# Kernel optimization log

Hardware: AMD Instinct MI355X
Metric: run time of the kernel (lower is better)

Reference implementation:

```python
import jax, jax.numpy as jnp
import numpy as np

B, N, FN, FE, H, FC, OUT = 64, 32, 32, 16, 32, 128, 1
ENN_LAYERS, S2S_STEPS = 3, 3


def setup_inputs() -> dict:
    key = jax.random.key(0)
    ks = jax.random.split(key, 16)
    s = 0.1
    return {
        "x": jax.random.uniform(ks[0], (B, N, FN), dtype=jnp.float32),
        "edge": jax.random.normal(ks[1], (B, N, N, FE), dtype=jnp.float32),
        "adjacency": jax.random.randint(ks[2], (B, N, N), 0, 2).astype(jnp.float32),
        # embedding layer
        "W_emb": s * jax.random.normal(ks[3], (FN, H)),
        "b_emb": jnp.zeros((H,), jnp.float32),
        # edge MLP: FE -> FC -> H*H
        "W1": s * jax.random.normal(ks[4], (FE, FC)),
        "b1": jnp.zeros((FC,), jnp.float32),
        "W2": s * jax.random.normal(ks[5], (FC, H * H)),
        "b2": jnp.zeros((H * H,), jnp.float32),
        # GRU (torch layout: weight_ih [3H,H], weight_hh [3H,H])
        "gru_Wi": s * jax.random.normal(ks[6], (3 * H, H)),
        "gru_Wh": s * jax.random.normal(ks[7], (3 * H, H)),
        "gru_bi": jnp.zeros((3 * H,), jnp.float32),
        "gru_bh": jnp.zeros((3 * H,), jnp.float32),
        # Set2Set LSTM: input 2H, hidden H (torch layout weight_ih [4H,2H])
        "lstm_Wi": s * jax.random.normal(ks[8], (4 * H, 2 * H)),
        "lstm_Wh": s * jax.random.normal(ks[9], (4 * H, H)),
        "lstm_bi": jnp.zeros((4 * H,), jnp.float32),
        "lstm_bh": jnp.zeros((4 * H,), jnp.float32),
        # output fc: 2H -> OUT
        "Wf": s * jax.random.normal(ks[10], (2 * H, OUT)),
        "bf": jnp.zeros((OUT,), jnp.float32),
    }


def reference(x, edge, adjacency, W_emb, b_emb, W1, b1, W2, b2,
              gru_Wi, gru_Wh, gru_bi, gru_bh,
              lstm_Wi, lstm_Wh, lstm_bi, lstm_bh, Wf, bf):
    Bx, Nx, _ = x.shape
    Hd = W_emb.shape[1]
    # node mask: (sum over raw features > 0), [B,N,1]
    msk = (jnp.sum(x, axis=2, keepdims=True) > 0).astype(x.dtype)
    h = x @ W_emb + b_emb  # [B,N,H]
    # per-edge weight matrices from edge MLP (same every layer in the original)
    ew = (jax.nn.relu(edge @ W1 + b1) @ W2 + b2).reshape(Bx, Nx, Nx, Hd, Hd)
    for _ in range(ENN_LAYERS):
        # msg[b,i,j,:] = ew[b,i,j] @ h[b,i]; masked by adjacency, summed over source i
        m = jnp.einsum('bijuv,biv->biju', ew, h) * adjacency[..., None]
        m = m.sum(axis=1)  # [B,N,H]
        # single-step GRU (torch gate order r,z,n)
        gi = m @ gru_Wi.T + gru_bi
        gh = h @ gru_Wh.T + gru_bh
        ir, iz, inn = jnp.split(gi, 3, axis=-1)
        hr, hz, hn = jnp.split(gh, 3, axis=-1)
        r = jax.nn.sigmoid(ir + hr)
        z = jax.nn.sigmoid(iz + hz)
        n = jnp.tanh(inn + r * hn)
        h = msk * ((1.0 - z) * n + z * h)
    # Set2Set readout (single-layer LSTM, torch gate order i,f,g,o)
    q = jnp.zeros((Bx, Hd), x.dtype)
    c = jnp.zeros((Bx, Hd), x.dtype)
    q_star = jnp.zeros((Bx, 2 * Hd), x.dtype)
    for _ in range(S2S_STEPS):
        g = q_star @ lstm_Wi.T + lstm_bi + q @ lstm_Wh.T + lstm_bh
        gi_, gf_, gg_, go_ = jnp.split(g, 4, axis=-1)
        c = jax.nn.sigmoid(gf_) * c + jax.nn.sigmoid(gi_) * jnp.tanh(gg_)
        q = jax.nn.sigmoid(go_) * jnp.tanh(c)
        e = jnp.einsum('bnh,bh->bn', h, q)
        e = jnp.where(msk[..., 0] == 0, -jnp.inf, e)
        a = jax.nn.softmax(e, axis=1)
        r = jnp.sum(a[..., None] * h * msk, axis=1)
        q_star = jnp.concatenate([q, r], axis=-1)
    return q_star @ Wf + bf  # [B,OUT]
```

## Files before the change

kernel.cpp:

```cpp
#include <hip/hip_runtime.h>
#include <hip/hip_bf16.h>
#include <math.h>

typedef __attribute__((ext_vector_type(8))) short bf16x8;
typedef __attribute__((ext_vector_type(16))) float f32x16;

__device__ __forceinline__ float sigf(float x) { return 1.0f / (1.0f + expf(-x)); }

__global__ __launch_bounds__(256, 4) void k_prep(
    const float* __restrict__ edge, const float* __restrict__ adj,
    const float* __restrict__ W1, const float* __restrict__ b1,
    const float* __restrict__ x, const float* __restrict__ W_emb,
    const float* __restrict__ b_emb, const float* __restrict__ W2,
    const float* __restrict__ gWi, const float* __restrict__ gWh,
    const float* __restrict__ b2, const float* __restrict__ lWi,
    const float* __restrict__ lWh,
    __hip_bfloat16* __restrict__ taT2, __hip_bfloat16* __restrict__ W2FTB,
    float* __restrict__ h, float* __restrict__ msk,
    float* __restrict__ gWiT, float* __restrict__ gWhT, float* __restrict__ b2T,
    float* __restrict__ lWiT, float* __restrict__ lWhT) {
    __shared__ float es[512];
    __shared__ float adjv[32];
    __shared__ float xs[256];
    __shared__ short t_lds[4096];
    const int tid = threadIdx.x, bid = blockIdx.x;
    const int b = bid >> 5, j = bid & 31;
    const int c = tid & 127, g = tid >> 7;
    float wr[16];
    #pragma unroll
    for (int v = 0; v < 16; ++v) wr[v] = W1[v * 128 + c];
    const float b1c = b1[c];
    if (tid < 128) {
        int i = tid >> 2, k4 = tid & 3;
        ((float4*)es)[tid] = *(const float4*)&edge[(((long)(b * 32 + i)) * 32 + j) * 16 + k4 * 4];
    } else if (tid < 160) {
        int i = tid - 128;
        adjv[i] = adj[(b * 32 + i) * 32 + j];
    }
    if (bid < 256) xs[tid] = x[bid * 256 + tid];
    __syncthreads();
    {
        #pragma unroll
        for (int ii = 0; ii < 16; ++ii) {
            int i = g * 16 + ii;
            const float* er = es + i * 16;
            float acc = b1c;
            #pragma unroll
            for (int k = 0; k < 16; ++k) acc += er[k] * wr[k];
            float val = adjv[i] * fmaxf(acc, 0.f);
            t_lds[c * 32 + i] = (short)__bfloat16_as_ushort(__float2bfloat16(val));
        }
    }
    __syncthreads();
    {
        int4* dst = (int4*)(taT2 + (long)bid * 4096);
        const int4* src = (const int4*)t_lds;
        dst[tid] = src[tid];
        dst[tid + 256] = src[tid + 256];
    }
    if (bid < 256) {
        int r = tid >> 5, u = tid & 31;
        int rowe = bid * 8 + r;
        float acc = b_emb[u];
        #pragma unroll
        for (int k = 0; k < 32; ++k) acc += xs[r * 32 + k] * W_emb[k * 32 + u];
        h[rowe * 32 + u] = acc;
        if (u == 0) {
            float s = 0.f;
            #pragma unroll
            for (int k = 0; k < 32; ++k) s += xs[r * 32 + k];
            msk[rowe] = (s > 0.f) ? 1.f : 0.f;
        }
    } else if (bid < 384) {
        int base = (bid - 256) * 1024;
        #pragma unroll
        for (int q = 0; q < 4; ++q) {
            int idx = base + q * 256 + tid;
            int chunk = idx >> 9, u = (idx >> 4) & 31, inner = idx & 15;
            int cv = chunk * 16 + inner;
            int cc = cv >> 5, v = cv & 31;
            W2FTB[idx] = __float2bfloat16(W2[cc * 1024 + u * 32 + v]);
        }
    } else if (bid == 384) {
        for (int idx = tid; idx < 3072; idx += 256) gWiT[(idx & 31) * 96 + (idx >> 5)] = gWi[idx];
        for (int idx = tid; idx < 3072; idx += 256) gWhT[(idx & 31) * 96 + (idx >> 5)] = gWh[idx];
        for (int idx = tid; idx < 1024; idx += 256) b2T[(idx & 31) * 32 + (idx >> 5)] = b2[idx];
        for (int idx = tid; idx < 8192; idx += 256) lWiT[(idx & 63) * 128 + (idx >> 6)] = lWi[idx];
        for (int idx = tid; idx < 4096; idx += 256) lWhT[(idx & 31) * 128 + (idx >> 5)] = lWh[idx];
    }
}

__global__ __launch_bounds__(256, 2) void k_msg(
    const __hip_bfloat16* __restrict__ taT2, const __hip_bfloat16* __restrict__ W2FTB,
    const float* __restrict__ h, float* __restrict__ partial) {
    __shared__ __align__(16) char P_lds[65536];
    __shared__ __align__(16) short hT[1024];
    const int tid = threadIdx.x, bid = blockIdx.x;
    const int b = bid >> 2, cq = bid & 3;
    const int w = tid >> 6, l = tid & 63, lid = l & 31, kh = l >> 5;
    for (int idx = tid; idx < 1024; idx += 256)
        hT[(idx & 31) * 32 + (idx >> 5)] =
            (short)__bfloat16_as_ushort(__float2bfloat16(h[b * 1024 + idx]));
    __syncthreads();
    const short* taB = (const short*)taT2 + (long)b * 131072;
    const short* w2b = (const short*)W2FTB;
    const short* hTp = hT + lid * 32 + kh * 8;
    bf16x8 hb0 = *(const bf16x8*)hTp;
    bf16x8 hb1 = *(const bf16x8*)(hTp + 16);
    #pragma unroll 2
    for (int q = 0; q < 8; ++q) {
        int jj = w * 8 + q;
        const short* ap = taB + (jj * 128 + cq * 32 + lid) * 32 + kh * 8;
        bf16x8 a0 = *(const bf16x8*)ap;
        bf16x8 a1 = *(const bf16x8*)(ap + 16);
        f32x16 accg = {};
        accg = __builtin_amdgcn_mfma_f32_32x32x16_bf16(a0, hb0, accg, 0, 0, 0);
        accg = __builtin_amdgcn_mfma_f32_32x32x16_bf16(a1, hb1, accg, 0, 0, 0);
        #pragma unroll
        for (int r = 0; r < 16; ++r) {
            int crow = (r & 3) + 8 * (r >> 2) + 4 * kh;
            int byte = (crow * 2 + (lid >> 4)) * 1024 + ((lid >> 3) & 1) * 512
                     + jj * 16 + (lid & 7) * 2;
            *(short*)(P_lds + byte) =
                (short)__bfloat16_as_ushort(__float2bfloat16(accg[r]));
        }
    }
    __syncthreads();
    f32x16 acc = {};
    #pragma unroll
    for (int kk = 0; kk < 16; ++kk) {
        int slice = w * 16 + kk;
        bf16x8 a = *(const bf16x8*)(P_lds + slice * 1024 + kh * 512 + lid * 16);
        bf16x8 bg = *(const bf16x8*)(w2b + (cq * 64 + slice) * 512 + lid * 16 + kh * 8);
        acc = __builtin_amdgcn_mfma_f32_32x32x16_bf16(a, bg, acc, 0, 0, 0);
    }
    __syncthreads();
    {
        float* red = (float*)P_lds + w * 1024;
        #pragma unroll
        for (int r = 0; r < 16; ++r) {
            int crow = (r & 3) + 8 * (r >> 2) + 4 * kh;
            red[crow * 32 + lid] = acc[r];
        }
    }
    __syncthreads();
    {
        float* r0 = (float*)P_lds;
        for (int k = tid; k < 1024; k += 256)
            partial[(long)bid * 1024 + k] = r0[k] + r0[1024 + k] + r0[2048 + k] + r0[3072 + k];
    }
}

__global__ __launch_bounds__(256, 2) void k_gru(
    const float* __restrict__ partial, const float* __restrict__ h,
    const float* __restrict__ adj, const float* __restrict__ msk,
    const float* __restrict__ b2T, const float* __restrict__ gWiT,
    const float* __restrict__ gWhT, const float* __restrict__ gbi,
    const float* __restrict__ gbh, float* __restrict__ hout) {
    __shared__ float hsh[1024], adjs[1024], wWiT[3072], wWhT[3072], b2s[1024];
    __shared__ float hsumL[256], mLs[256], gbs[192];
    const int tid = threadIdx.x, bid = blockIdx.x;
    const int b = bid >> 2, jc = bid & 3;
    const int j8 = tid >> 5, u = tid & 31, jg = jc * 8 + j8;
    for (int k = tid; k < 1024; k += 256) hsh[k] = h[b * 1024 + k];
    for (int k = tid; k < 1024; k += 256) adjs[k] = adj[b * 1024 + k];
    for (int k = tid; k < 3072; k += 256) wWiT[k] = gWiT[k];
    for (int k = tid; k < 3072; k += 256) wWhT[k] = gWhT[k];
    for (int k = tid; k < 1024; k += 256) b2s[k] = b2T[k];
    if (tid < 96) gbs[tid] = gbi[tid];
    else if (tid < 192) gbs[tid] = gbh[tid - 96];
    float ps = 0.f;
    #pragma unroll
    for (int cq = 0; cq < 4; ++cq)
        ps += partial[((long)(b * 4 + cq)) * 1024 + jc * 256 + tid];
    __syncthreads();
    float hs = 0.f;
    #pragma unroll
    for (int i = 0; i < 32; ++i) hs += adjs[i * 32 + jg] * hsh[i * 32 + u];
    hsumL[tid] = hs;
    __syncthreads();
    float m = ps;
    #pragma unroll
    for (int v = 0; v < 32; ++v) m += b2s[v * 32 + u] * hsumL[j8 * 32 + v];
    mLs[tid] = m;
    __syncthreads();
    float gi[3], gh[3];
    #pragma unroll
    for (int kb = 0; kb < 3; ++kb) {
        int k = kb * 32 + u;
        float a = gbs[k], c = gbs[96 + k];
        #pragma unroll
        for (int v = 0; v < 32; ++v) {
            a += mLs[j8 * 32 + v] * wWiT[v * 96 + k];
            c += hsh[jg * 32 + v] * wWhT[v * 96 + k];
        }
        gi[kb] = a; gh[kb] = c;
    }
    float r = sigf(gi[0] + gh[0]);
    float z = sigf(gi[1] + gh[1]);
    float n = tanhf(gi[2] + r * gh[2]);
    float hv = hsh[jg * 32 + u];
    float mm = msk[b * 32 + jg];
    float res = mm * ((1.f - z) * n + z * hv);
    hout[b * 1024 + jg * 32 + u] = res;
}

__global__ __launch_bounds__(128, 4) void k_s2s(
    const float* __restrict__ h, const float* __restrict__ msk,
    const float* __restrict__ lWiT, const float* __restrict__ lWhT,
    const float* __restrict__ lbi, const float* __restrict__ lbh,
    const float* __restrict__ Wf, const float* __restrict__ bf,
    float* __restrict__ out) {
    __shared__ float hsh[1024];
    __shared__ float mskk[32], qs[32], cs2[32], qstar[64], gsv[128], asv[32];
    const int tid = threadIdx.x, b = blockIdx.x;
    for (int k = tid; k < 1024; k += 128) hsh[k] = h[b * 1024 + k];
    if (tid < 32) { mskk[tid] = msk[b * 32 + tid]; qs[tid] = 0.f; cs2[tid] = 0.f; }
    if (tid < 64) qstar[tid] = 0.f;
    __syncthreads();
    for (int step = 0; step < 3; ++step) {
        {
            float g = lbi[tid] + lbh[tid];
            #pragma unroll
            for (int pp = 0; pp < 64; ++pp) g += qstar[pp] * lWiT[pp * 128 + tid];
            #pragma unroll
            for (int v = 0; v < 32; ++v) g += qs[v] * lWhT[v * 128 + tid];
            gsv[tid] = g;
        }
        __syncthreads();
        if (tid < 32) {
            float ci = sigf(gsv[32 + tid]) * cs2[tid] + sigf(gsv[tid]) * tanhf(gsv[64 + tid]);
            cs2[tid] = ci;
            qs[tid] = sigf(gsv[96 + tid]) * tanhf(ci);
        }
        __syncthreads();
        if (tid < 32) {
            float e = 0.f;
            #pragma unroll
            for (int v = 0; v < 32; ++v) e += hsh[tid * 32 + v] * qs[v];
            e = (mskk[tid] == 0.f) ? -INFINITY : e;
            float mx = e;
            for (int o = 16; o >= 1; o >>= 1) mx = fmaxf(mx, __shfl_xor(mx, o, 64));
            float a = expf(e - mx);
            float ss = a;
            for (int o = 16; o >= 1; o >>= 1) ss += __shfl_xor(ss, o, 64);
            asv[tid] = a / ss;
        }
        __syncthreads();
        if (tid < 32) {
            float rr = 0.f;
            #pragma unroll
            for (int nn = 0; nn < 32; ++nn) rr += asv[nn] * hsh[nn * 32 + tid] * mskk[nn];
            qstar[tid] = qs[tid];
            qstar[32 + tid] = rr;
        }
        __syncthreads();
    }
    if (tid < 64) {
        float v = qstar[tid] * Wf[tid];
        for (int o = 32; o >= 1; o >>= 1) v += __shfl_xor(v, o, 64);
        if (tid == 0) out[b] = v + bf[0];
    }
}

extern "C" void kernel_launch(void* const* d_in, const int* in_sizes, int n_in,
                              void* d_out, int out_size, void* d_ws, size_t ws_size,
                              hipStream_t stream) {
    const float* x    = (const float*)d_in[0];
    const float* edge = (const float*)d_in[1];
    const float* adj  = (const float*)d_in[2];
    const float* W_emb= (const float*)d_in[3];
    const float* b_emb= (const float*)d_in[4];
    const float* W1   = (const float*)d_in[5];
    const float* b1   = (const float*)d_in[6];
    const float* W2   = (const float*)d_in[7];
    const float* b2   = (const float*)d_in[8];
    const float* gWi  = (const float*)d_in[9];
    const float* gWh  = (const float*)d_in[10];
    const float* gbi  = (const float*)d_in[11];
    const float* gbh  = (const float*)d_in[12];
    const float* lWi  = (const float*)d_in[13];
    const float* lWh  = (const float*)d_in[14];
    const float* lbi  = (const float*)d_in[15];
    const float* lbh  = (const float*)d_in[16];
    const float* Wf   = (const float*)d_in[17];
    const float* bf   = (const float*)d_in[18];
    float* out = (float*)d_out;

    __hip_bfloat16* taT2  = (__hip_bfloat16*)d_ws;
    __hip_bfloat16* W2FTB = taT2 + 8388608;
    float* hA   = (float*)(W2FTB + 131072);
    float* hB   = hA + 65536;
    float* mskp = hB + 65536;
    float* partial = mskp + 2048;
    float* gWiT = partial + 262144;
    float* gWhT = gWiT + 3072;
    float* b2T  = gWhT + 3072;
    float* lWiT = b2T + 1024;
    float* lWhT = lWiT + 8192;

    k_prep<<<2048, 256, 0, stream>>>(edge, adj, W1, b1, x, W_emb, b_emb, W2,
                                     gWi, gWh, b2, lWi, lWh,
                                     taT2, W2FTB, hA, mskp,
                                     gWiT, gWhT, b2T, lWiT, lWhT);
    float* hcur = hA; float* hnxt = hB;
    for (int l = 0; l < 3; ++l) {
        k_msg<<<256, 256, 0, stream>>>(taT2, W2FTB, hcur, partial);
        k_gru<<<256, 256, 0, stream>>>(partial, hcur, adj, mskp, b2T,
                                       gWiT, gWhT, gbi, gbh, hnxt);
        float* tf = hcur; hcur = hnxt; hnxt = tf;
    }
    k_s2s<<<64, 128, 0, stream>>>(hcur, mskp, lWiT, lWhT, lbi, lbh, Wf, bf, out);
}
```

Baseline: 101.8 us.

## Fuse message, GRU and Set2Set into one per-graph layer kernel

```diff
diff --git a/kernel.cpp b/kernel.cpp
--- a/kernel.cpp
+++ b/kernel.cpp
@@ -6,6 +6,7 @@
 typedef __attribute__((ext_vector_type(16))) float f32x16;
 
 __device__ __forceinline__ float sigf(float x) { return 1.0f / (1.0f + expf(-x)); }
+__device__ __forceinline__ int swz(int b) { return b ^ ((b >> 5) & 0x30) ^ ((b >> 7) & 0x40); }
 
 __global__ __launch_bounds__(256, 4) void k_prep(
     const float* __restrict__ edge, const float* __restrict__ adj,
@@ -90,51 +91,87 @@
     }
 }
 
-__global__ __launch_bounds__(256, 2) void k_msg(
+__global__ __launch_bounds__(512, 1) void k_layer(
     const __hip_bfloat16* __restrict__ taT2, const __hip_bfloat16* __restrict__ W2FTB,
-    const float* __restrict__ h, float* __restrict__ partial) {
+    const float* __restrict__ hin, float* __restrict__ hout,
+    const float* __restrict__ adj, const float* __restrict__ msk,
+    const float* __restrict__ gWiT, const float* __restrict__ gWhT,
+    const float* __restrict__ b2T, const float* __restrict__ gbi,
+    const float* __restrict__ gbh,
+    const float* __restrict__ lWiT, const float* __restrict__ lWhT,
+    const float* __restrict__ lbi, const float* __restrict__ lbh,
+    const float* __restrict__ Wf, const float* __restrict__ bf,
+    float* __restrict__ out, int final_) {
     __shared__ __align__(16) char P_lds[65536];
     __shared__ __align__(16) short hT[1024];
-    const int tid = threadIdx.x, bid = blockIdx.x;
-    const int b = bid >> 2, cq = bid & 3;
+    __shared__ float hsh[1024], adjs[1024];
+    __shared__ float wWiT[3104], wWhT[3104];
+    __shared__ float b2s[1056];
+    __shared__ float gbs[192];
+    __shared__ float hsumL[1024], mLs[1024];
+    __shared__ float mskk[32], qs[32], cs2[32], qstar[64], gsv[128], asv[32];
+
+    const int tid = threadIdx.x, b = blockIdx.x;
     const int w = tid >> 6, l = tid & 63, lid = l & 31, kh = l >> 5;
-    for (int idx = tid; idx < 1024; idx += 256)
-        hT[(idx & 31) * 32 + (idx >> 5)] =
-            (short)__bfloat16_as_ushort(__float2bfloat16(h[b * 1024 + idx]));
-    __syncthreads();
+    const int j16 = tid >> 5, u = tid & 31;
+
+    {
+        #pragma unroll
+        for (int p = 0; p < 2; ++p) {
+            int idx = tid + p * 512;
+            float hv = hin[b * 1024 + idx];
+            hsh[idx] = hv;
+            hT[(idx & 31) * 32 + (idx >> 5)] = (short)__bfloat16_as_ushort(__float2bfloat16(hv));
+            adjs[idx] = adj[b * 1024 + idx];
+        }
+        for (int idx = tid; idx < 3072; idx += 512) {
+            int v = idx / 96, k = idx % 96;
+            wWiT[v * 97 + k] = gWiT[idx];
+            wWhT[v * 97 + k] = gWhT[idx];
+        }
+        for (int idx = tid; idx < 1024; idx += 512)
+            b2s[(idx >> 5) * 33 + (idx & 31)] = b2T[idx];
+        if (tid < 96) gbs[tid] = gbi[tid];
+        else if (tid < 192) gbs[tid] = gbh[tid - 96];
+        if (tid < 32) mskk[tid] = msk[b * 32 + tid];
+    }
+    __syncthreads();
+
     const short* taB = (const short*)taT2 + (long)b * 131072;
     const short* w2b = (const short*)W2FTB;
     const short* hTp = hT + lid * 32 + kh * 8;
     bf16x8 hb0 = *(const bf16x8*)hTp;
     bf16x8 hb1 = *(const bf16x8*)(hTp + 16);
-    #pragma unroll 2
-    for (int q = 0; q < 8; ++q) {
-        int jj = w * 8 + q;
-        const short* ap = taB + (jj * 128 + cq * 32 + lid) * 32 + kh * 8;
-        bf16x8 a0 = *(const bf16x8*)ap;
-        bf16x8 a1 = *(const bf16x8*)(ap + 16);
-        f32x16 accg = {};
-        accg = __builtin_amdgcn_mfma_f32_32x32x16_bf16(a0, hb0, accg, 0, 0, 0);
-        accg = __builtin_amdgcn_mfma_f32_32x32x16_bf16(a1, hb1, accg, 0, 0, 0);
-        #pragma unroll
-        for (int r = 0; r < 16; ++r) {
-            int crow = (r & 3) + 8 * (r >> 2) + 4 * kh;
-            int byte = (crow * 2 + (lid >> 4)) * 1024 + ((lid >> 3) & 1) * 512
-                     + jj * 16 + (lid & 7) * 2;
-            *(short*)(P_lds + byte) =
-                (short)__bfloat16_as_ushort(__float2bfloat16(accg[r]));
-        }
-    }
-    __syncthreads();
     f32x16 acc = {};
-    #pragma unroll
-    for (int kk = 0; kk < 16; ++kk) {
-        int slice = w * 16 + kk;
-        bf16x8 a = *(const bf16x8*)(P_lds + slice * 1024 + kh * 512 + lid * 16);
-        bf16x8 bg = *(const bf16x8*)(w2b + (cq * 64 + slice) * 512 + lid * 16 + kh * 8);
-        acc = __builtin_amdgcn_mfma_f32_32x32x16_bf16(a, bg, acc, 0, 0, 0);
-    }
-    __syncthreads();
+    for (int cq = 0; cq < 4; ++cq) {
+        #pragma unroll
+        for (int q = 0; q < 4; ++q) {
+            int jj = w * 4 + q;
+            const short* ap = taB + (jj * 128 + cq * 32 + lid) * 32 + kh * 8;
+            bf16x8 a0 = *(const bf16x8*)ap;
+            bf16x8 a1 = *(const bf16x8*)(ap + 16);
+            f32x16 accg = {};
+            accg = __builtin_amdgcn_mfma_f32_32x32x16_bf16(a0, hb0, accg, 0, 0, 0);
+            accg = __builtin_amdgcn_mfma_f32_32x32x16_bf16(a1, hb1, accg, 0, 0, 0);
+            #pragma unroll
+            for (int r = 0; r < 16; ++r) {
+                int crow = (r & 3) + 8 * (r >> 2) + 4 * kh;
+                int byte = (crow * 2 + (lid >> 4)) * 1024 + ((lid >> 3) & 1) * 512
+                         + jj * 16 + (lid & 7) * 2;
+                *(short*)(P_lds + swz(byte)) =
+                    (short)__bfloat16_as_ushort(__float2bfloat16(accg[r]));
+            }
+        }
+        __syncthreads();
+        #pragma unroll
+        for (int kk = 0; kk < 8; ++kk) {
+            int slice = w * 8 + kk;
+            bf16x8 a = *(const bf16x8*)(P_lds + swz(slice * 1024 + kh * 512 + lid * 16));
+            bf16x8 bg = *(const bf16x8*)(w2b + (cq * 64 + slice) * 512 + lid * 16 + kh * 8);
+            acc = __builtin_amdgcn_mfma_f32_32x32x16_bf16(a, bg, acc, 0, 0, 0);
+        }
+        __syncthreads();
+    }
     {
         float* red = (float*)P_lds + w * 1024;
         #pragma unroll
@@ -144,82 +181,67 @@
         }
     }
     __syncthreads();
-    {
-        float* r0 = (float*)P_lds;
-        for (int k = tid; k < 1024; k += 256)
-            partial[(long)bid * 1024 + k] = r0[k] + r0[1024 + k] + r0[2048 + k] + r0[3072 + k];
-    }
-}
-
-__global__ __launch_bounds__(256, 2) void k_gru(
-    const float* __restrict__ partial, const float* __restrict__ h,
-    const float* __restrict__ adj, const float* __restrict__ msk,
-    const float* __restrict__ b2T, const float* __restrict__ gWiT,
-    const float* __restrict__ gWhT, const float* __restrict__ gbi,
-    const float* __restrict__ gbh, float* __restrict__ hout) {
-    __shared__ float hsh[1024], adjs[1024], wWiT[3072], wWhT[3072], b2s[1024];
-    __shared__ float hsumL[256], mLs[256], gbs[192];
-    const int tid = threadIdx.x, bid = blockIdx.x;
-    const int b = bid >> 2, jc = bid & 3;
-    const int j8 = tid >> 5, u = tid & 31, jg = jc * 8 + j8;
-    for (int k = tid; k < 1024; k += 256) hsh[k] = h[b * 1024 + k];
-    for (int k = tid; k < 1024; k += 256) adjs[k] = adj[b * 1024 + k];
-    for (int k = tid; k < 3072; k += 256) wWiT[k] = gWiT[k];
-    for (int k = tid; k < 3072; k += 256) wWhT[k] = gWhT[k];
-    for (int k = tid; k < 1024; k += 256) b2s[k] = b2T[k];
-    if (tid < 96) gbs[tid] = gbi[tid];
-    else if (tid < 192) gbs[tid] = gbh[tid - 96];
-    float ps = 0.f;
+    float res[2];
+    {
+        float ps[2];
+        #pragma unroll
+        for (int p = 0; p < 2; ++p) {
+            float s = 0.f;
+            #pragma unroll
+            for (int w8 = 0; w8 < 8; ++w8) s += ((float*)P_lds)[w8 * 1024 + p * 512 + tid];
+            ps[p] = s;
+        }
+        #pragma unroll
+        for (int p = 0; p < 2; ++p) {
+            int j = j16 + p * 16;
+            float hs = 0.f;
+            #pragma unroll
+            for (int i = 0; i < 32; ++i) hs += adjs[i * 32 + j] * hsh[i * 32 + u];
+            hsumL[p * 512 + tid] = hs;
+        }
+        __syncthreads();
+        #pragma unroll
+        for (int p = 0; p < 2; ++p) {
+            float m = ps[p];
+            #pragma unroll
+            for (int v = 0; v < 32; ++v) m += b2s[v * 33 + u] * hsumL[p * 512 + j16 * 32 + v];
+            mLs[p * 512 + tid] = m;
+        }
+        __syncthreads();
+        #pragma unroll
+        for (int p = 0; p < 2; ++p) {
+            int j = j16 + p * 16;
+            float gi[3], gh[3];
+            #pragma unroll
+            for (int kb = 0; kb < 3; ++kb) {
+                int k = kb * 32 + u;
+                float a = gbs[k], cgh = gbs[96 + k];
+                #pragma unroll
+                for (int v = 0; v < 32; ++v) {
+                    a   += mLs[p * 512 + j16 * 32 + v] * wWiT[v * 97 + k];
+                    cgh += hsh[j * 32 + v] * wWhT[v * 97 + k];
+                }
+                gi[kb] = a; gh[kb] = cgh;
+            }
+            float r = sigf(gi[0] + gh[0]);
+            float z = sigf(gi[1] + gh[1]);
+            float n = tanhf(gi[2] + r * gh[2]);
+            float hv = hsh[j * 32 + u];
+            res[p] = mskk[j] * ((1.f - z) * n + z * hv);
+        }
+    }
+    __syncthreads();
     #pragma unroll
-    for (int cq = 0; cq < 4; ++cq)
-        ps += partial[((long)(b * 4 + cq)) * 1024 + jc * 256 + tid];
-    __syncthreads();
-    float hs = 0.f;
-    #pragma unroll
-    for (int i = 0; i < 32; ++i) hs += adjs[i * 32 + jg] * hsh[i * 32 + u];
-    hsumL[tid] = hs;
-    __syncthreads();
-    float m = ps;
-    #pragma unroll
-    for (int v = 0; v < 32; ++v) m += b2s[v * 32 + u] * hsumL[j8 * 32 + v];
-    mLs[tid] = m;
-    __syncthreads();
-    float gi[3], gh[3];
-    #pragma unroll
-    for (int kb = 0; kb < 3; ++kb) {
-        int k = kb * 32 + u;
-        float a = gbs[k], c = gbs[96 + k];
-        #pragma unroll
-        for (int v = 0; v < 32; ++v) {
-            a += mLs[j8 * 32 + v] * wWiT[v * 96 + k];
-            c += hsh[jg * 32 + v] * wWhT[v * 96 + k];
-        }
-        gi[kb] = a; gh[kb] = c;
-    }
-    float r = sigf(gi[0] + gh[0]);
-    float z = sigf(gi[1] + gh[1]);
-    float n = tanhf(gi[2] + r * gh[2]);
-    float hv = hsh[jg * 32 + u];
-    float mm = msk[b * 32 + jg];
-    float res = mm * ((1.f - z) * n + z * hv);
-    hout[b * 1024 + jg * 32 + u] = res;
-}
-
-__global__ __launch_bounds__(128, 4) void k_s2s(
-    const float* __restrict__ h, const float* __restrict__ msk,
-    const float* __restrict__ lWiT, const float* __restrict__ lWhT,
-    const float* __restrict__ lbi, const float* __restrict__ lbh,
-    const float* __restrict__ Wf, const float* __restrict__ bf,
-    float* __restrict__ out) {
-    __shared__ float hsh[1024];
-    __shared__ float mskk[32], qs[32], cs2[32], qstar[64], gsv[128], asv[32];
-    const int tid = threadIdx.x, b = blockIdx.x;
-    for (int k = tid; k < 1024; k += 128) hsh[k] = h[b * 1024 + k];
-    if (tid < 32) { mskk[tid] = msk[b * 32 + tid]; qs[tid] = 0.f; cs2[tid] = 0.f; }
-    if (tid < 64) qstar[tid] = 0.f;
+    for (int p = 0; p < 2; ++p) {
+        int j = j16 + p * 16;
+        hsh[j * 32 + u] = res[p];
+        hout[b * 1024 + j * 32 + u] = res[p];
+    }
+    if (!final_) return;
+    if (tid < 64) { qstar[tid] = 0.f; if (tid < 32) { qs[tid] = 0.f; cs2[tid] = 0.f; } }
     __syncthreads();
     for (int step = 0; step < 3; ++step) {
-        {
+        if (tid < 128) {
             float g = lbi[tid] + lbh[tid];
             #pragma unroll
             for (int pp = 0; pp < 64; ++pp) g += qstar[pp] * lWiT[pp * 128 + tid];
@@ -292,8 +314,7 @@
     float* hA   = (float*)(W2FTB + 131072);
     float* hB   = hA + 65536;
     float* mskp = hB + 65536;
-    float* partial = mskp + 2048;
-    float* gWiT = partial + 262144;
+    float* gWiT = mskp + 2048;
     float* gWhT = gWiT + 3072;
     float* b2T  = gWhT + 3072;
     float* lWiT = b2T + 1024;
@@ -305,10 +326,10 @@
                                      gWiT, gWhT, b2T, lWiT, lWhT);
     float* hcur = hA; float* hnxt = hB;
     for (int l = 0; l < 3; ++l) {
-        k_msg<<<256, 256, 0, stream>>>(taT2, W2FTB, hcur, partial);
-        k_gru<<<256, 256, 0, stream>>>(partial, hcur, adj, mskp, b2T,
-                                       gWiT, gWhT, gbi, gbh, hnxt);
+        k_layer<<<64, 512, 0, stream>>>(taT2, W2FTB, hcur, hnxt, adj, mskp,
+                                        gWiT, gWhT, b2T, gbi, gbh,
+                                        lWiT, lWhT, lbi, lbh, Wf, bf, out,
+                                        (l == 2) ? 1 : 0);
         float* tf = hcur; hcur = hnxt; hnxt = tf;
     }
-    k_s2s<<<64, 128, 0, stream>>>(hcur, mskp, lWiT, lWhT, lbi, lbh, Wf, bf, out);
 }
```

New measurement: 207.0 us. +103.3%, slower.

## Fuse message and GRU kernels per layer by repartitioning work over target nodes

Applied to the files above, without the earlier changes.

```diff
diff --git a/kernel.cpp b/kernel.cpp
--- a/kernel.cpp
+++ b/kernel.cpp
@@ -16,7 +16,7 @@
     const float* __restrict__ b2, const float* __restrict__ lWi,
     const float* __restrict__ lWh,
     __hip_bfloat16* __restrict__ taT2, __hip_bfloat16* __restrict__ W2FTB,
-    float* __restrict__ h, float* __restrict__ msk,
+    float* __restrict__ h, short* __restrict__ hTg, float* __restrict__ msk,
     float* __restrict__ gWiT, float* __restrict__ gWhT, float* __restrict__ b2T,
     float* __restrict__ lWiT, float* __restrict__ lWhT) {
     __shared__ float es[512];
@@ -65,6 +65,8 @@
         #pragma unroll
         for (int k = 0; k < 32; ++k) acc += xs[r * 32 + k] * W_emb[k * 32 + u];
         h[rowe * 32 + u] = acc;
+        hTg[(rowe >> 5) * 1024 + u * 32 + (rowe & 31)] =
+            (short)__bfloat16_as_ushort(__float2bfloat16(acc));
         if (u == 0) {
             float s = 0.f;
             #pragma unroll
@@ -90,27 +92,39 @@
     }
 }
 
-__global__ __launch_bounds__(256, 2) void k_msg(
+__global__ __launch_bounds__(256, 2) void k_layer(
     const __hip_bfloat16* __restrict__ taT2, const __hip_bfloat16* __restrict__ W2FTB,
-    const float* __restrict__ h, float* __restrict__ partial) {
+    const float* __restrict__ hin, const short* __restrict__ hTin,
+    float* __restrict__ hout, short* __restrict__ hTout,
+    const float* __restrict__ adj, const float* __restrict__ msk,
+    const float* __restrict__ gWiT, const float* __restrict__ gWhT,
+    const float* __restrict__ b2T, const float* __restrict__ gbi,
+    const float* __restrict__ gbh) {
     __shared__ __align__(16) char P_lds[65536];
     __shared__ __align__(16) short hT[1024];
+    __shared__ float hsh[1024], adjs[1024];
+    __shared__ float hsumL[256], gbs[192], mskk[32];
     const int tid = threadIdx.x, bid = blockIdx.x;
-    const int b = bid >> 2, cq = bid & 3;
+    const int b = bid >> 2, jc = bid & 3;
     const int w = tid >> 6, l = tid & 63, lid = l & 31, kh = l >> 5;
-    for (int idx = tid; idx < 1024; idx += 256)
-        hT[(idx & 31) * 32 + (idx >> 5)] =
-            (short)__bfloat16_as_ushort(__float2bfloat16(h[b * 1024 + idx]));
-    __syncthreads();
-    const short* taB = (const short*)taT2 + (long)b * 131072;
+
+    if (tid < 128) ((int4*)hT)[tid] = ((const int4*)(hTin + b * 1024))[tid];
+    for (int k = tid; k < 1024; k += 256) { hsh[k] = hin[b * 1024 + k]; adjs[k] = adj[b * 1024 + k]; }
+    if (tid < 96) gbs[tid] = gbi[tid];
+    else if (tid < 192) gbs[tid] = gbh[tid - 96];
+    if (tid < 32) mskk[tid] = msk[b * 32 + tid];
+    __syncthreads();
+
+    const short* taB = (const short*)taT2 + (long)b * 131072 + jc * 8 * 128 * 32;
     const short* w2b = (const short*)W2FTB;
     const short* hTp = hT + lid * 32 + kh * 8;
     bf16x8 hb0 = *(const bf16x8*)hTp;
     bf16x8 hb1 = *(const bf16x8*)(hTp + 16);
     #pragma unroll 2
     for (int q = 0; q < 8; ++q) {
-        int jj = w * 8 + q;
-        const short* ap = taB + (jj * 128 + cq * 32 + lid) * 32 + kh * 8;
+        int t = w * 8 + q;
+        int jj = t >> 2, cbase = (t & 3) * 32;
+        const short* ap = taB + ((jj * 128 + cbase + lid) * 32 + kh * 8);
         bf16x8 a0 = *(const bf16x8*)ap;
         bf16x8 a1 = *(const bf16x8*)(ap + 16);
         f32x16 accg = {};
@@ -119,90 +133,65 @@
         #pragma unroll
         for (int r = 0; r < 16; ++r) {
             int crow = (r & 3) + 8 * (r >> 2) + 4 * kh;
-            int byte = (crow * 2 + (lid >> 4)) * 1024 + ((lid >> 3) & 1) * 512
-                     + jj * 16 + (lid & 7) * 2;
+            int byte = (jj * 8192 + (cbase + crow) * 64 + lid * 2) ^ (jj << 4);
             *(short*)(P_lds + byte) =
                 (short)__bfloat16_as_ushort(__float2bfloat16(accg[r]));
         }
     }
     __syncthreads();
     f32x16 acc = {};
-    #pragma unroll
-    for (int kk = 0; kk < 16; ++kk) {
-        int slice = w * 16 + kk;
-        bf16x8 a = *(const bf16x8*)(P_lds + slice * 1024 + kh * 512 + lid * 16);
-        bf16x8 bg = *(const bf16x8*)(w2b + (cq * 64 + slice) * 512 + lid * 16 + kh * 8);
+    const int jloc = lid & 7;
+    #pragma unroll 4
+    for (int step = 0; step < 64; ++step) {
+        int abyte = (jloc * 8192 + w * 2048 + step * 32 + kh * 16) ^ (jloc << 4);
+        bf16x8 a = *(const bf16x8*)(P_lds + abyte);
+        bf16x8 bg = *(const bf16x8*)(w2b + (w * 64 + step) * 512 + lid * 16 + kh * 8);
         acc = __builtin_amdgcn_mfma_f32_32x32x16_bf16(a, bg, acc, 0, 0, 0);
     }
     __syncthreads();
-    {
-        float* red = (float*)P_lds + w * 1024;
-        #pragma unroll
-        for (int r = 0; r < 16; ++r) {
-            int crow = (r & 3) + 8 * (r >> 2) + 4 * kh;
-            red[crow * 32 + lid] = acc[r];
-        }
-    }
-    __syncthreads();
-    {
-        float* r0 = (float*)P_lds;
-        for (int k = tid; k < 1024; k += 256)
-            partial[(long)bid * 1024 + k] = r0[k] + r0[1024 + k] + r0[2048 + k] + r0[3072 + k];
-    }
-}
-
-__global__ __launch_bounds__(256, 2) void k_gru(
-    const float* __restrict__ partial, const float* __restrict__ h,
-    const float* __restrict__ adj, const float* __restrict__ msk,
-    const float* __restrict__ b2T, const float* __restrict__ gWiT,
-    const float* __restrict__ gWhT, const float* __restrict__ gbi,
-    const float* __restrict__ gbh, float* __restrict__ hout) {
-    __shared__ float hsh[1024], adjs[1024], wWiT[3072], wWhT[3072], b2s[1024];
-    __shared__ float hsumL[256], mLs[256], gbs[192];
-    const int tid = threadIdx.x, bid = blockIdx.x;
-    const int b = bid >> 2, jc = bid & 3;
+    float* mred = (float*)P_lds;
+    float* wWiT = (float*)P_lds + 1024;
+    float* wWhT = (float*)P_lds + 4096;
+    float* b2s  = (float*)P_lds + 7168;
+    float* mLs  = (float*)P_lds + 8192;
+    #pragma unroll
+    for (int r = 0; r < 4; ++r)
+        mred[w * 256 + (4 * kh + r) * 32 + lid] = acc[r];
+    for (int k = tid; k < 3072; k += 256) { wWiT[k] = gWiT[k]; wWhT[k] = gWhT[k]; }
+    for (int k = tid; k < 1024; k += 256) b2s[k] = b2T[k];
+    __syncthreads();
     const int j8 = tid >> 5, u = tid & 31, jg = jc * 8 + j8;
-    for (int k = tid; k < 1024; k += 256) hsh[k] = h[b * 1024 + k];
-    for (int k = tid; k < 1024; k += 256) adjs[k] = adj[b * 1024 + k];
-    for (int k = tid; k < 3072; k += 256) wWiT[k] = gWiT[k];
-    for (int k = tid; k < 3072; k += 256) wWhT[k] = gWhT[k];
-    for (int k = tid; k < 1024; k += 256) b2s[k] = b2T[k];
-    if (tid < 96) gbs[tid] = gbi[tid];
-    else if (tid < 192) gbs[tid] = gbh[tid - 96];
-    float ps = 0.f;
-    #pragma unroll
-    for (int cq = 0; cq < 4; ++cq)
-        ps += partial[((long)(b * 4 + cq)) * 1024 + jc * 256 + tid];
-    __syncthreads();
+    float msum = mred[j8 * 32 + u] + mred[256 + j8 * 32 + u]
+               + mred[512 + j8 * 32 + u] + mred[768 + j8 * 32 + u];
     float hs = 0.f;
     #pragma unroll
     for (int i = 0; i < 32; ++i) hs += adjs[i * 32 + jg] * hsh[i * 32 + u];
     hsumL[tid] = hs;
     __syncthreads();
-    float m = ps;
+    float m = msum;
     #pragma unroll
     for (int v = 0; v < 32; ++v) m += b2s[v * 32 + u] * hsumL[j8 * 32 + v];
-    mLs[tid] = m;
+    mLs[j8 * 32 + u] = m;
     __syncthreads();
     float gi[3], gh[3];
     #pragma unroll
     for (int kb = 0; kb < 3; ++kb) {
         int k = kb * 32 + u;
-        float a = gbs[k], c = gbs[96 + k];
+        float a = gbs[k], cgh = gbs[96 + k];
         #pragma unroll
         for (int v = 0; v < 32; ++v) {
-            a += mLs[j8 * 32 + v] * wWiT[v * 96 + k];
-            c += hsh[jg * 32 + v] * wWhT[v * 96 + k];
-        }
-        gi[kb] = a; gh[kb] = c;
+            a   += mLs[j8 * 32 + v] * wWiT[v * 96 + k];
+            cgh += hsh[jg * 32 + v] * wWhT[v * 96 + k];
+        }
+        gi[kb] = a; gh[kb] = cgh;
     }
     float r = sigf(gi[0] + gh[0]);
     float z = sigf(gi[1] + gh[1]);
     float n = tanhf(gi[2] + r * gh[2]);
     float hv = hsh[jg * 32 + u];
-    float mm = msk[b * 32 + jg];
-    float res = mm * ((1.f - z) * n + z * hv);
+    float res = mskk[jg] * ((1.f - z) * n + z * hv);
     hout[b * 1024 + jg * 32 + u] = res;
+    hTout[b * 1024 + u * 32 + jg] = (short)__bfloat16_as_ushort(__float2bfloat16(res));
 }
 
 __global__ __launch_bounds__(128, 4) void k_s2s(
@@ -289,11 +278,12 @@
 
     __hip_bfloat16* taT2  = (__hip_bfloat16*)d_ws;
     __hip_bfloat16* W2FTB = taT2 + 8388608;
-    float* hA   = (float*)(W2FTB + 131072);
+    short* hTgA = (short*)(W2FTB + 131072);
+    short* hTgB = hTgA + 65536;
+    float* hA   = (float*)(hTgB + 65536);
     float* hB   = hA + 65536;
     float* mskp = hB + 65536;
-    float* partial = mskp + 2048;
-    float* gWiT = partial + 262144;
+    float* gWiT = mskp + 2048;
     float* gWhT = gWiT + 3072;
     float* b2T  = gWhT + 3072;
     float* lWiT = b2T + 1024;
@@ -301,14 +291,15 @@
 
     k_prep<<<2048, 256, 0, stream>>>(edge, adj, W1, b1, x, W_emb, b_emb, W2,
                                      gWi, gWh, b2, lWi, lWh,
-                                     taT2, W2FTB, hA, mskp,
+                                     taT2, W2FTB, hA, hTgA, mskp,
                                      gWiT, gWhT, b2T, lWiT, lWhT);
     float* hcur = hA; float* hnxt = hB;
+    short* hTcur = hTgA; short* hTnxt = hTgB;
     for (int l = 0; l < 3; ++l) {
-        k_msg<<<256, 256, 0, stream>>>(taT2, W2FTB, hcur, partial);
-        k_gru<<<256, 256, 0, stream>>>(partial, hcur, adj, mskp, b2T,
-                                       gWiT, gWhT, gbi, gbh, hnxt);
+        k_layer<<<256, 256, 0, stream>>>(taT2, W2FTB, hcur, hTcur, hnxt, hTnxt,
+                                         adj, mskp, gWiT, gWhT, b2T, gbi, gbh);
         float* tf = hcur; hcur = hnxt; hnxt = tf;
+        short* ts = hTcur; hTcur = hTnxt; hTnxt = ts;
     }
     k_s2s<<<64, 128, 0, stream>>>(hcur, mskp, lWiT, lWhT, lbi, lbh, Wf, bf, out);
 }
```

Measured after the change: 108.1 us. 1.06x slower.

## Fuse final GRU layer with Set2Set readout and swizzle k_msg LDS layout

Applied to the files above, without the earlier changes.

```diff
diff --git a/kernel.cpp b/kernel.cpp
--- a/kernel.cpp
+++ b/kernel.cpp
@@ -6,6 +6,7 @@
 typedef __attribute__((ext_vector_type(16))) float f32x16;
 
 __device__ __forceinline__ float sigf(float x) { return 1.0f / (1.0f + expf(-x)); }
+__device__ __forceinline__ int swz(int b) { return b ^ ((b >> 5) & 0x30) ^ ((b >> 7) & 0x40); }
 
 __global__ __launch_bounds__(256, 4) void k_prep(
     const float* __restrict__ edge, const float* __restrict__ adj,
@@ -13,12 +14,10 @@
     const float* __restrict__ x, const float* __restrict__ W_emb,
     const float* __restrict__ b_emb, const float* __restrict__ W2,
     const float* __restrict__ gWi, const float* __restrict__ gWh,
-    const float* __restrict__ b2, const float* __restrict__ lWi,
-    const float* __restrict__ lWh,
+    const float* __restrict__ b2,
     __hip_bfloat16* __restrict__ taT2, __hip_bfloat16* __restrict__ W2FTB,
     float* __restrict__ h, float* __restrict__ msk,
-    float* __restrict__ gWiT, float* __restrict__ gWhT, float* __restrict__ b2T,
-    float* __restrict__ lWiT, float* __restrict__ lWhT) {
+    float* __restrict__ gWiT, float* __restrict__ gWhT, float* __restrict__ b2T) {
     __shared__ float es[512];
     __shared__ float adjv[32];
     __shared__ float xs[256];
@@ -85,8 +84,6 @@
         for (int idx = tid; idx < 3072; idx += 256) gWiT[(idx & 31) * 96 + (idx >> 5)] = gWi[idx];
         for (int idx = tid; idx < 3072; idx += 256) gWhT[(idx & 31) * 96 + (idx >> 5)] = gWh[idx];
         for (int idx = tid; idx < 1024; idx += 256) b2T[(idx & 31) * 32 + (idx >> 5)] = b2[idx];
-        for (int idx = tid; idx < 8192; idx += 256) lWiT[(idx & 63) * 128 + (idx >> 6)] = lWi[idx];
-        for (int idx = tid; idx < 4096; idx += 256) lWhT[(idx & 31) * 128 + (idx >> 5)] = lWh[idx];
     }
 }
 
@@ -110,7 +107,7 @@
     #pragma unroll 2
     for (int q = 0; q < 8; ++q) {
         int jj = w * 8 + q;
-        const short* ap = taB + (jj * 128 + cq * 32 + lid) * 32 + kh * 8;
+        const short* ap = taB + ((jj * 128 + cq * 32 + lid) * 32 + kh * 8);
         bf16x8 a0 = *(const bf16x8*)ap;
         bf16x8 a1 = *(const bf16x8*)(ap + 16);
         f32x16 accg = {};
@@ -121,7 +118,7 @@
             int crow = (r & 3) + 8 * (r >> 2) + 4 * kh;
             int byte = (crow * 2 + (lid >> 4)) * 1024 + ((lid >> 3) & 1) * 512
                      + jj * 16 + (lid & 7) * 2;
-            *(short*)(P_lds + byte) =
+            *(short*)(P_lds + swz(byte)) =
                 (short)__bfloat16_as_ushort(__float2bfloat16(accg[r]));
         }
     }
@@ -130,7 +127,7 @@
     #pragma unroll
     for (int kk = 0; kk < 16; ++kk) {
         int slice = w * 16 + kk;
-        bf16x8 a = *(const bf16x8*)(P_lds + slice * 1024 + kh * 512 + lid * 16);
+        bf16x8 a = *(const bf16x8*)(P_lds + swz(slice * 1024 + kh * 512 + lid * 16));
         bf16x8 bg = *(const bf16x8*)(w2b + (cq * 64 + slice) * 512 + lid * 16 + kh * 8);
         acc = __builtin_amdgcn_mfma_f32_32x32x16_bf16(a, bg, acc, 0, 0, 0);
     }
@@ -201,30 +198,82 @@
     float n = tanhf(gi[2] + r * gh[2]);
     float hv = hsh[jg * 32 + u];
     float mm = msk[b * 32 + jg];
-    float res = mm * ((1.f - z) * n + z * hv);
-    hout[b * 1024 + jg * 32 + u] = res;
-}
-
-__global__ __launch_bounds__(128, 4) void k_s2s(
-    const float* __restrict__ h, const float* __restrict__ msk,
-    const float* __restrict__ lWiT, const float* __restrict__ lWhT,
+    hout[b * 1024 + jg * 32 + u] = mm * ((1.f - z) * n + z * hv);
+}
+
+__global__ __launch_bounds__(1024, 1) void k_gru_final(
+    const float* __restrict__ partial, const float* __restrict__ h,
+    const float* __restrict__ adj, const float* __restrict__ msk,
+    const float* __restrict__ gWi, const float* __restrict__ gWh,
+    const float* __restrict__ gbi, const float* __restrict__ gbh,
+    const float* __restrict__ b2,
+    const float* __restrict__ lWi, const float* __restrict__ lWh,
     const float* __restrict__ lbi, const float* __restrict__ lbh,
     const float* __restrict__ Wf, const float* __restrict__ bf,
     float* __restrict__ out) {
-    __shared__ float hsh[1024];
+    __shared__ float hsh[1024], adjs[1024];
+    __shared__ float wWiT[3104], wWhT[3104];
+    __shared__ float b2s[1056];
+    __shared__ float gbs[192];
+    __shared__ float hsumL[1024], mLs[1024];
     __shared__ float mskk[32], qs[32], cs2[32], qstar[64], gsv[128], asv[32];
     const int tid = threadIdx.x, b = blockIdx.x;
-    for (int k = tid; k < 1024; k += 128) hsh[k] = h[b * 1024 + k];
-    if (tid < 32) { mskk[tid] = msk[b * 32 + tid]; qs[tid] = 0.f; cs2[tid] = 0.f; }
-    if (tid < 64) qstar[tid] = 0.f;
+    const int j = tid >> 5, u = tid & 31;
+    {
+        hsh[tid] = h[b * 1024 + tid];
+        adjs[tid] = adj[b * 1024 + tid];
+        if (tid < 32) mskk[tid] = msk[b * 32 + tid];
+        for (int idx = tid; idx < 3072; idx += 1024)
+            wWiT[(idx & 31) * 97 + (idx >> 5)] = gWi[idx];
+        for (int idx = tid; idx < 3072; idx += 1024)
+            wWhT[(idx & 31) * 97 + (idx >> 5)] = gWh[idx];
+        if (tid < 96) gbs[tid] = gbi[tid];
+        else if (tid < 192) gbs[tid] = gbh[tid - 96];
+        b2s[(tid & 31) * 33 + (tid >> 5)] = b2[tid];
+    }
+    float ps = 0.f;
+    #pragma unroll
+    for (int cq = 0; cq < 4; ++cq)
+        ps += partial[((long)(b * 4 + cq)) * 1024 + tid];
+    __syncthreads();
+    float hs = 0.f;
+    #pragma unroll
+    for (int i = 0; i < 32; ++i) hs += adjs[i * 32 + j] * hsh[i * 32 + u];
+    hsumL[tid] = hs;
+    __syncthreads();
+    float m = ps;
+    #pragma unroll
+    for (int v = 0; v < 32; ++v) m += b2s[v * 33 + u] * hsumL[j * 32 + v];
+    mLs[tid] = m;
+    __syncthreads();
+    float gi[3], gh[3];
+    #pragma unroll
+    for (int kb = 0; kb < 3; ++kb) {
+        int k = kb * 32 + u;
+        float a = gbs[k], cgh = gbs[96 + k];
+        #pragma unroll
+        for (int v = 0; v < 32; ++v) {
+            a   += mLs[j * 32 + v] * wWiT[v * 97 + k];
+            cgh += hsh[j * 32 + v] * wWhT[v * 97 + k];
+        }
+        gi[kb] = a; gh[kb] = cgh;
+    }
+    float r = sigf(gi[0] + gh[0]);
+    float z = sigf(gi[1] + gh[1]);
+    float n = tanhf(gi[2] + r * gh[2]);
+    float hv = hsh[tid];
+    float res = mskk[j] * ((1.f - z) * n + z * hv);
+    hsumL[tid] = res;
+    float* hn = hsumL;
+    if (tid < 64) { qstar[tid] = 0.f; if (tid < 32) { qs[tid] = 0.f; cs2[tid] = 0.f; } }
     __syncthreads();
     for (int step = 0; step < 3; ++step) {
-        {
+        if (tid < 128) {
             float g = lbi[tid] + lbh[tid];
             #pragma unroll
-            for (int pp = 0; pp < 64; ++pp) g += qstar[pp] * lWiT[pp * 128 + tid];
-            #pragma unroll
-            for (int v = 0; v < 32; ++v) g += qs[v] * lWhT[v * 128 + tid];
+            for (int pp = 0; pp < 64; ++pp) g += qstar[pp] * lWi[tid * 64 + pp];
+            #pragma unroll
+            for (int v = 0; v < 32; ++v) g += qs[v] * lWh[tid * 32 + v];
             gsv[tid] = g;
         }
         __syncthreads();
@@ -237,7 +286,7 @@
         if (tid < 32) {
             float e = 0.f;
             #pragma unroll
-            for (int v = 0; v < 32; ++v) e += hsh[tid * 32 + v] * qs[v];
+            for (int v = 0; v < 32; ++v) e += hn[tid * 32 + v] * qs[v];
             e = (mskk[tid] == 0.f) ? -INFINITY : e;
             float mx = e;
             for (int o = 16; o >= 1; o >>= 1) mx = fmaxf(mx, __shfl_xor(mx, o, 64));
@@ -250,7 +299,7 @@
         if (tid < 32) {
             float rr = 0.f;
             #pragma unroll
-            for (int nn = 0; nn < 32; ++nn) rr += asv[nn] * hsh[nn * 32 + tid] * mskk[nn];
+            for (int nn = 0; nn < 32; ++nn) rr += asv[nn] * hn[nn * 32 + tid] * mskk[nn];
             qstar[tid] = qs[tid];
             qstar[32 + tid] = rr;
         }
@@ -296,19 +345,19 @@
     float* gWiT = partial + 262144;
     float* gWhT = gWiT + 3072;
     float* b2T  = gWhT + 3072;
-    float* lWiT = b2T + 1024;
-    float* lWhT = lWiT + 8192;
 
     k_prep<<<2048, 256, 0, stream>>>(edge, adj, W1, b1, x, W_emb, b_emb, W2,
-                                     gWi, gWh, b2, lWi, lWh,
-                                     taT2, W2FTB, hA, mskp,
-                                     gWiT, gWhT, b2T, lWiT, lWhT);
+                                     gWi, gWh, b2,
+                                     taT2, W2FTB, hA, mskp, gWiT, gWhT, b2T);
     float* hcur = hA; float* hnxt = hB;
-    for (int l = 0; l < 3; ++l) {
+    for (int l = 0; l < 2; ++l) {
         k_msg<<<256, 256, 0, stream>>>(taT2, W2FTB, hcur, partial);
         k_gru<<<256, 256, 0, stream>>>(partial, hcur, adj, mskp, b2T,
                                        gWiT, gWhT, gbi, gbh, hnxt);
         float* tf = hcur; hcur = hnxt; hnxt = tf;
     }
-    k_s2s<<<64, 128, 0, stream>>>(hcur, mskp, lWiT, lWhT, lbi, lbh, Wf, bf, out);
-}
+    k_msg<<<256, 256, 0, stream>>>(taT2, W2FTB, hcur, partial);
+    k_gru_final<<<64, 1024, 0, stream>>>(partial, hcur, adj, mskp,
+                                         gWi, gWh, gbi, gbh, b2,
+                                         lWi, lWh, lbi, lbh, Wf, bf, out);
+}
```

Measured after the change: 104.8 us. 1.03x slower.
